# Performance work log

Measured on AMD Instinct MI355X. Metric: run time of the kernel, lower is better.

The kernel has to match this reference:

```python
import jax, jax.numpy as jnp
import numpy as np

B, S, E = 2, 4096, 768
NH, D = 12, 64
W = 256            # one-sided attention window (attention_window=512 // 2)
NEG = jnp.float32(-1e30)  # stands in for -inf at invalid band positions (safe grads)


def setup_inputs() -> dict:
    key = jax.random.key(0)
    ks = jax.random.split(key, 4)
    sc = 0.02
    return {
        'hidden_states': jax.random.normal(ks[0], (B, S, E), jnp.float32),
        'attention_mask': jnp.zeros((B, S), jnp.float32),   # 0 = local attention everywhere
        'is_index_masked': jnp.zeros((B, S), bool),
        'Wq': jax.random.normal(ks[1], (E, E), jnp.float32) * sc,
        'bq': jnp.zeros((E,), jnp.float32),
        'Wk': jax.random.normal(ks[2], (E, E), jnp.float32) * sc,
        'bk': jnp.zeros((E,), jnp.float32),
        'Wv': jax.random.normal(ks[3], (E, E), jnp.float32) * sc,
        'bv': jnp.zeros((E,), jnp.float32),
    }


def _longformer_local(hidden_states, attention_mask, is_index_masked, Wq, bq, Wk, bk, Wv, bv):
    b, s, e = hidden_states.shape
    w = W
    nc = s // w
    # projections (nn.Linear: x @ W.T + b); query pre-scaled by 1/sqrt(head_dim)
    q = (hidden_states @ Wq.T + bq) / jnp.sqrt(jnp.float32(D))
    k = hidden_states @ Wk.T + bk
    v = hidden_states @ Wv.T + bv
    # [B, NH, S, D]
    q = q.reshape(b, s, NH, D).transpose(0, 2, 1, 3)
    k = k.reshape(b, s, NH, D).transpose(0, 2, 1, 3)
    v = v.reshape(b, s, NH, D).transpose(0, 2, 1, 3)

    # pad keys/values by w on each side; chunk into [B,NH,nc,3w,D] windows
    kp = jnp.pad(k, ((0, 0), (0, 0), (w, w), (0, 0)))
    vp = jnp.pad(v, ((0, 0), (0, 0), (w, w), (0, 0)))
    starts = jnp.arange(nc) * w                      # [nc]
    cidx = starts[:, None] + jnp.arange(3 * w)[None, :]  # [nc, 3w] (padded coords)
    kc = kp[:, :, cidx, :]                            # [B,NH,nc,3w,D]
    vc = vp[:, :, cidx, :]                            # [B,NH,nc,3w,D]
    qc = q.reshape(b, NH, nc, w, D)

    # banded scores: query p in chunk attends keys at offsets p..p+2w within the 3w window
    scores = jnp.einsum('bhcpd,bhckd->bhcpk', qc, kc)  # [B,NH,nc,w,3w]
    p = jnp.arange(w)[:, None]
    koff = jnp.arange(2 * w + 1)[None, :]
    band_idx = p + koff                                # [w, 2w+1]
    band = jnp.take_along_axis(scores, band_idx[None, None, None], axis=-1)  # [B,NH,nc,w,2w+1]

    # additive mask from attention_mask (torch: finfo.min where !=0), gathered at key positions
    fmask = jnp.where(attention_mask != 0, jnp.finfo(jnp.float32).min, jnp.float32(0.0))  # [B,S]
    j = starts[:, None, None] + band_idx[None] - w     # global key index [nc,w,2w+1]
    valid = (j >= 0) & (j < s)
    jc = jnp.clip(j, 0, s - 1)
    band = band + fmask[:, jc][:, None]                # [B,1->NH,nc,w,2w+1]
    # _mask_invalid_locations: out-of-sequence band entries -> -inf (NEG)
    band = jnp.where(valid[None, None], band, NEG)

    probs = jax.nn.softmax(band.astype(jnp.float32), axis=-1)
    # zero probs at fully-masked query positions
    im = is_index_masked.reshape(b, 1, nc, w, 1)
    probs = jnp.where(im, jnp.float32(0.0), probs)

    # scatter band back to [B,NH,nc,w,3w] and contract with value chunks
    full = jnp.zeros((b, NH, nc, w, 3 * w), probs.dtype).at[:, :, :, p, band_idx].set(probs)
    out = jnp.einsum('bhcpk,bhckd->bhcpd', full, vc)   # [B,NH,nc,w,D]
    out = out.reshape(b, NH, s, D).transpose(0, 2, 1, 3).reshape(b, s, e)
    return out


def reference(hidden_states, attention_mask, is_index_masked, Wq, bq, Wk, bk, Wv, bv):
    return _longformer_local(hidden_states, attention_mask, is_index_masked,
                             Wq, bq, Wk, bk, Wv, bv)
```

## Files before the change

### kernel.cpp

```cpp
#include <hip/hip_runtime.h>

typedef __bf16 bf16;
typedef __attribute__((ext_vector_type(8))) __bf16 bf16x8;
typedef __attribute__((ext_vector_type(4))) __bf16 bf16x4;
typedef __attribute__((ext_vector_type(4))) float f32x4;

#define MFMA16(a, b, c) __builtin_amdgcn_mfma_f32_16x16x32_bf16((a), (b), (c), 0, 0, 0)

#define S_LEN 4096
#define NHEAD 12
#define EMB   768
#define NEGV  (-1e30f)

__device__ __forceinline__ void gload16(const bf16* g, bf16* l) {
  __builtin_amdgcn_global_load_lds((const __attribute__((address_space(1))) void*)g,
                                   (__attribute__((address_space(3))) void*)l, 16, 0, 0);
}

__global__ __launch_bounds__(256) void cvt_kernel(const float* __restrict__ x,
                                                  bf16* __restrict__ o, int n8, float scale) {
  int i = blockIdx.x * 256 + threadIdx.x;
  if (i >= n8) return;
  const float4* p = (const float4*)(x + (size_t)i * 8);
  float4 a = p[0], b = p[1];
  bf16x8 v;
  v[0] = (bf16)(a.x * scale); v[1] = (bf16)(a.y * scale);
  v[2] = (bf16)(a.z * scale); v[3] = (bf16)(a.w * scale);
  v[4] = (bf16)(b.x * scale); v[5] = (bf16)(b.y * scale);
  v[6] = (bf16)(b.z * scale); v[7] = (bf16)(b.w * scale);
  *(bf16x8*)(o + (size_t)i * 8) = v;
}

__global__ __launch_bounds__(256) void cvt3_kernel(const float* __restrict__ w0,
                                                   const float* __restrict__ w1,
                                                   const float* __restrict__ w2,
                                                   bf16* __restrict__ o, int n8) {
  int which = blockIdx.y;
  const float* src = (which == 0) ? w0 : (which == 1) ? w1 : w2;
  float scale = (which == 0) ? 0.125f : 1.0f;
  int i = blockIdx.x * 256 + threadIdx.x;
  if (i >= n8) return;
  const float4* p = (const float4*)(src + (size_t)i * 8);
  float4 a = p[0], b = p[1];
  bf16x8 v;
  v[0] = (bf16)(a.x * scale); v[1] = (bf16)(a.y * scale);
  v[2] = (bf16)(a.z * scale); v[3] = (bf16)(a.w * scale);
  v[4] = (bf16)(b.x * scale); v[5] = (bf16)(b.y * scale);
  v[6] = (bf16)(b.z * scale); v[7] = (bf16)(b.w * scale);
  *(bf16x8*)(o + ((size_t)which * n8 + i) * 8) = v;
}

__global__ __launch_bounds__(256) void qkv_gemm(const bf16* __restrict__ Xb, const bf16* __restrict__ Wb,
                                                const float* __restrict__ bq, const float* __restrict__ bk,
                                                const float* __restrict__ bv,
                                                bf16* __restrict__ Qo, bf16* __restrict__ Ko,
                                                bf16* __restrict__ Vt) {
  __shared__ union SM {
    struct { bf16 a[128 * 64]; bf16 b[128 * 64]; } st;
    bf16 c[128 * 130];
  } sm;
  const int tid = threadIdx.x;
  const int l = tid & 63, w = tid >> 6;
  const int ln = l & 15, g = l >> 4;
  const int wm = w >> 1, wn = w & 1;
  const int m0 = blockIdx.x * 128;
  const int n0 = blockIdx.y * 128;

  const f32x4 zero4 = {0.f, 0.f, 0.f, 0.f};
  f32x4 acc[4][4];
#pragma unroll
  for (int i = 0; i < 4; ++i)
#pragma unroll
    for (int j = 0; j < 4; ++j) acc[i][j] = zero4;

  for (int kt = 0; kt < 12; ++kt) {
    const int k0 = kt * 64;
#pragma unroll
    for (int i = 0; i < 4; ++i) {
      const int G = w * 256 + i * 64 + l;
      const int row = G >> 3, dsl = G & 7;
      const int slot = dsl ^ (row & 7);
      gload16(Xb + (size_t)(m0 + row) * 768 + k0 + slot * 8, &sm.st.a[(w * 256 + i * 64) * 8]);
      gload16(Wb + (size_t)(n0 + row) * 768 + k0 + slot * 8, &sm.st.b[(w * 256 + i * 64) * 8]);
    }
    asm volatile("s_waitcnt vmcnt(0)" ::: "memory");
    __syncthreads();
#pragma unroll
    for (int kc = 0; kc < 2; ++kc) {
      bf16x8 af[4], bfr[4];
#pragma unroll
      for (int i = 0; i < 4; ++i) {
        int ra = wm * 64 + i * 16 + ln;
        af[i] = *(const bf16x8*)(&sm.st.a[ra * 64 + ((kc * 4 + g) ^ (ra & 7)) * 8]);
        int rb = wn * 64 + i * 16 + ln;
        bfr[i] = *(const bf16x8*)(&sm.st.b[rb * 64 + ((kc * 4 + g) ^ (rb & 7)) * 8]);
      }
#pragma unroll
      for (int mi = 0; mi < 4; ++mi)
#pragma unroll
        for (int ni = 0; ni < 4; ++ni)
          acc[mi][ni] = MFMA16(af[mi], bfr[ni], acc[mi][ni]);
    }
    __syncthreads();
  }

  const int which = n0 / 768;
  const int h0 = (n0 % 768) >> 6;
  const int b = m0 >> 12;
  const int h = h0 + wn;
  const float bsc = (which == 0) ? 0.125f : 1.0f;
  const float* bias = (which == 0) ? bq : (which == 1) ? bk : bv;
  float bvv[4];
#pragma unroll
  for (int ni = 0; ni < 4; ++ni) bvv[ni] = bias[h * 64 + ni * 16 + ln] * bsc;

  if (which < 2) {
    bf16* dst = (which == 0) ? Qo : Ko;
    const size_t base = ((size_t)(b * NHEAD + h) * S_LEN + (m0 & 4095)) * 64;
#pragma unroll
    for (int mi = 0; mi < 4; ++mi)
#pragma unroll
      for (int ni = 0; ni < 4; ++ni)
#pragma unroll
        for (int r = 0; r < 4; ++r) {
          int sl = wm * 64 + mi * 16 + g * 4 + r;
          dst[base + (size_t)sl * 64 + ni * 16 + ln] = (bf16)(acc[mi][ni][r] + bvv[ni]);
        }
  } else {
#pragma unroll
    for (int mi = 0; mi < 4; ++mi)
#pragma unroll
      for (int ni = 0; ni < 4; ++ni)
#pragma unroll
        for (int r = 0; r < 4; ++r) {
          int sl = wm * 64 + mi * 16 + g * 4 + r;
          sm.c[sl * 130 + wn * 64 + ni * 16 + ln] = (bf16)(acc[mi][ni][r] + bvv[ni]);
        }
    __syncthreads();
#pragma unroll
    for (int it = 0; it < 4; ++it) {
      int d = it * 32 + (tid >> 3);
      int scp = tid & 7;
      int hh = h0 + (d >> 6);
      bf16x8 o0, o1;
#pragma unroll
      for (int i2 = 0; i2 < 8; ++i2) o0[i2] = sm.c[(scp * 16 + i2) * 130 + d];
#pragma unroll
      for (int i2 = 0; i2 < 8; ++i2) o1[i2] = sm.c[(scp * 16 + 8 + i2) * 130 + d];
      bf16* dp = Vt + ((size_t)(b * NHEAD + hh) * 64 + (d & 63)) * S_LEN + (m0 & 4095) + scp * 16;
      *(bf16x8*)dp = o0;
      *(bf16x8*)(dp + 8) = o1;
    }
  }
}

__global__ __launch_bounds__(512) void attn_kernel(const bf16* __restrict__ Qb, const bf16* __restrict__ Kb,
                                                   const bf16* __restrict__ Vtb,
                                                   const float* __restrict__ amask,
                                                   const unsigned char* __restrict__ imask,
                                                   float* __restrict__ out) {
  __shared__ bf16 Ks[2][64 * 64];
  __shared__ bf16 Vs[2][64 * 64];
  __shared__ bf16 Pt[8][16 * 64];
  __shared__ float Ams[2][64];
  const int tid = threadIdx.x;
  const int l = tid & 63, w = tid >> 6;
  const int ln = l & 15, g = l >> 4;
  const int orig = blockIdx.x;
  const int lb = (orig & 7) * 96 + (orig >> 3);
  const int qc = lb & 31, bh = lb >> 5;
  const int b = bh / NHEAD, h = bh % NHEAD;
  const int q0 = qc * 128;
  const int qg = q0 + w * 16 + ln;

  const size_t qoff = ((size_t)bh * S_LEN + qg) * 64;
  const bf16x8 qf0 = *(const bf16x8*)(Qb + qoff + g * 8);
  const bf16x8 qf1 = *(const bf16x8*)(Qb + qoff + 32 + g * 8);

  const f32x4 zero4 = {0.f, 0.f, 0.f, 0.f};
  f32x4 acc[4];
#pragma unroll
  for (int i = 0; i < 4; ++i) acc[i] = zero4;
  float mrun = -1e38f, lrun = 0.f;

  const int t_lo = (q0 >= 256) ? 0 : ((256 - q0) >> 6);
  int t_hi = (S_LEN + 256 - q0) >> 6;
  if (t_hi > 10) t_hi = 10;

  auto stage = [&](int sb, int t) {
    const int tj0 = q0 - 256 + t * 64;
    const int G = w * 64 + l;
    const int row = G >> 3, dsl = G & 7;
    const int slot = dsl ^ (row & 7);
    gload16(Kb + ((size_t)bh * S_LEN + tj0 + row) * 64 + slot * 8, &Ks[sb][w * 512]);
    gload16(Vtb + ((size_t)bh * 64 + row) * S_LEN + tj0 + slot * 8, &Vs[sb][w * 512]);
    if (tid < 64) {
      float am = amask[b * S_LEN + tj0 + tid];
      Ams[sb][tid] = (am != 0.f) ? -1e30f : 0.f;
    }
  };

  stage(0, t_lo);
  asm volatile("s_waitcnt vmcnt(0)" ::: "memory");
  __syncthreads();

  int buf = 0;
  for (int t = t_lo; t < t_hi; ++t, buf ^= 1) {
    if (t + 1 < t_hi) stage(buf ^ 1, t + 1);
    const int tj0 = q0 - 256 + t * 64;

    f32x4 sc[4];
#pragma unroll
    for (int i = 0; i < 4; ++i) sc[i] = zero4;
    __builtin_amdgcn_s_setprio(1);
#pragma unroll
    for (int kc = 0; kc < 2; ++kc) {
      bf16x8 qf = kc ? qf1 : qf0;
#pragma unroll
      for (int mi = 0; mi < 4; ++mi) {
        int r = mi * 16 + ln;
        bf16x8 kf = *(const bf16x8*)(&Ks[buf][r * 64 + ((kc * 4 + g) ^ (r & 7)) * 8]);
        sc[mi] = MFMA16(kf, qf, sc[mi]);
      }
    }
    __builtin_amdgcn_s_setprio(0);

    float mt = -1e38f;
    const bool full = (t * 64 >= w * 16 + 15) && (t * 64 <= w * 16 + 449);
    if (full) {
#pragma unroll
      for (int mi = 0; mi < 4; ++mi)
#pragma unroll
        for (int r = 0; r < 4; ++r) {
          int key = mi * 16 + g * 4 + r;
          float v = sc[mi][r] + Ams[buf][key];
          sc[mi][r] = v;
          mt = fmaxf(mt, v);
        }
    } else {
#pragma unroll
      for (int mi = 0; mi < 4; ++mi)
#pragma unroll
        for (int r = 0; r < 4; ++r) {
          int key = mi * 16 + g * 4 + r;
          int j = tj0 + key;
          bool valid = (j >= qg - 256) && (j <= qg + 256);
          float v = valid ? (sc[mi][r] + Ams[buf][key]) : NEGV;
          sc[mi][r] = v;
          mt = fmaxf(mt, v);
        }
    }
    mt = fmaxf(mt, __shfl_xor(mt, 16));
    mt = fmaxf(mt, __shfl_xor(mt, 32));
    if (!__all(mt <= mrun + 8.f)) {
      float mnew = fmaxf(mrun, mt);
      float corr = __expf(mrun - mnew);
      lrun *= corr;
#pragma unroll
      for (int i = 0; i < 4; ++i) acc[i] *= corr;
      mrun = mnew;
    }
    float psum = 0.f;
    float pv[4][4];
#pragma unroll
    for (int mi = 0; mi < 4; ++mi)
#pragma unroll
      for (int r = 0; r < 4; ++r) {
        float p = __expf(sc[mi][r] - mrun);
        pv[mi][r] = p;
        psum += p;
      }
    psum += __shfl_xor(psum, 16);
    psum += __shfl_xor(psum, 32);
    lrun += psum;

    bf16* PtW = &Pt[w][0];
#pragma unroll
    for (int mi = 0; mi < 4; ++mi) {
      bf16x4 pk;
      pk[0] = (bf16)pv[mi][0]; pk[1] = (bf16)pv[mi][1];
      pk[2] = (bf16)pv[mi][2]; pk[3] = (bf16)pv[mi][3];
      *(bf16x4*)(&PtW[ln * 64 + ((mi * 4 + g) ^ ln) * 4]) = pk;
    }

    __builtin_amdgcn_s_setprio(1);
#pragma unroll
    for (int ds2 = 0; ds2 < 4; ++ds2) {
#pragma unroll
      for (int kc = 0; kc < 2; ++kc) {
        int r = ds2 * 16 + ln;
        bf16x8 vf = *(const bf16x8*)(&Vs[buf][r * 64 + ((kc * 4 + g) ^ (r & 7)) * 8]);
        bf16x4 pa = *(const bf16x4*)(&PtW[ln * 64 + ((kc * 8 + g * 2) ^ ln) * 4]);
        bf16x4 pb = *(const bf16x4*)(&PtW[ln * 64 + ((kc * 8 + g * 2 + 1) ^ ln) * 4]);
        bf16x8 pf = __builtin_shufflevector(pa, pb, 0, 1, 2, 3, 4, 5, 6, 7);
        acc[ds2] = MFMA16(vf, pf, acc[ds2]);
      }
    }
    __builtin_amdgcn_s_setprio(0);

    asm volatile("s_waitcnt vmcnt(0)" ::: "memory");
    __syncthreads();
  }

  float rl = 1.0f / lrun;
  if (imask[b * S_LEN + qg] != 0) rl = 0.0f;
  float* ob = out + ((size_t)b * S_LEN + qg) * EMB + h * 64;
#pragma unroll
  for (int ds2 = 0; ds2 < 4; ++ds2) {
    float4 o;
    o.x = acc[ds2][0] * rl; o.y = acc[ds2][1] * rl;
    o.z = acc[ds2][2] * rl; o.w = acc[ds2][3] * rl;
    *(float4*)(ob + ds2 * 16 + g * 4) = o;
  }
}

extern "C" void kernel_launch(void* const* d_in, const int* in_sizes, int n_in,
                              void* d_out, int out_size, void* d_ws, size_t ws_size,
                              hipStream_t stream) {
  const float* X = (const float*)d_in[0];
  const float* amask = (const float*)d_in[1];
  const unsigned char* imask = (const unsigned char*)d_in[2];
  const float* Wq = (const float*)d_in[3];
  const float* bq = (const float*)d_in[4];
  const float* Wk = (const float*)d_in[5];
  const float* bk = (const float*)d_in[6];
  const float* Wv = (const float*)d_in[7];
  const float* bv = (const float*)d_in[8];
  float* out = (float*)d_out;

  bf16* Xb = (bf16*)d_ws;
  bf16* Wb = Xb + 6291456;
  bf16* Qb = Wb + 3 * 589824;
  bf16* Kb = Qb + 6291456;
  bf16* Vt = Kb + 6291456;

  cvt_kernel<<<3072, 256, 0, stream>>>(X, Xb, 6291456 / 8, 1.0f);
  cvt3_kernel<<<dim3(288, 3), 256, 0, stream>>>(Wq, Wk, Wv, Wb, 589824 / 8);
  qkv_gemm<<<dim3(64, 18), 256, 0, stream>>>(Xb, Wb, bq, bk, bv, Qb, Kb, Vt);
  attn_kernel<<<768, 512, 0, stream>>>(Qb, Kb, Vt, amask, imask, out);
}
```

Baseline: 186.3 us.

## Double-buffer QKV GEMM LDS tiles and stage Q/K epilogue through LDS

The QKV projection GEMM now keeps two LDS buffers for the A and B tiles. It issues the global-to-LDS loads for the next K-step before computing on the current one, so memory latency can overlap with MFMA work. The Q/K epilogue now also goes through the shared C tile, turning scattered 2-byte global stores into 16-byte row-contiguous writes. In exchange, LDS use doubles, which can lower occupancy. The explicit vmcnt wait was removed, so correctness relies on the barrier draining the async loads. The 130-element row pitch also makes the 16-byte LDS reads misaligned.

```diff
diff --git a/kernel.cpp b/kernel.cpp
--- a/kernel.cpp
+++ b/kernel.cpp
@@ -56,7 +56,7 @@
                                                 bf16* __restrict__ Qo, bf16* __restrict__ Ko,
                                                 bf16* __restrict__ Vt) {
   __shared__ union SM {
-    struct { bf16 a[128 * 64]; bf16 b[128 * 64]; } st;
+    struct { bf16 a[2][128 * 64]; bf16 b2[2][128 * 64]; } st;
     bf16 c[128 * 130];
   } sm;
   const int tid = threadIdx.x;
@@ -73,27 +73,38 @@
 #pragma unroll
     for (int j = 0; j < 4; ++j) acc[i][j] = zero4;
 
-  for (int kt = 0; kt < 12; ++kt) {
+  int srow[4], sslot[4];
+#pragma unroll
+  for (int i = 0; i < 4; ++i) {
+    const int G = w * 256 + i * 64 + l;
+    srow[i] = G >> 3;
+    sslot[i] = (G & 7) ^ (srow[i] & 7);
+  }
+
+  auto stage = [&](int sb, int kt) {
     const int k0 = kt * 64;
 #pragma unroll
     for (int i = 0; i < 4; ++i) {
-      const int G = w * 256 + i * 64 + l;
-      const int row = G >> 3, dsl = G & 7;
-      const int slot = dsl ^ (row & 7);
-      gload16(Xb + (size_t)(m0 + row) * 768 + k0 + slot * 8, &sm.st.a[(w * 256 + i * 64) * 8]);
-      gload16(Wb + (size_t)(n0 + row) * 768 + k0 + slot * 8, &sm.st.b[(w * 256 + i * 64) * 8]);
-    }
-    asm volatile("s_waitcnt vmcnt(0)" ::: "memory");
-    __syncthreads();
+      gload16(Xb + (size_t)(m0 + srow[i]) * 768 + k0 + sslot[i] * 8, &sm.st.a[sb][(w * 256 + i * 64) * 8]);
+      gload16(Wb + (size_t)(n0 + srow[i]) * 768 + k0 + sslot[i] * 8, &sm.st.b2[sb][(w * 256 + i * 64) * 8]);
+    }
+  };
+
+  stage(0, 0);
+  __syncthreads();
+
+  int buf = 0;
+  for (int kt = 0; kt < 12; ++kt, buf ^= 1) {
+    if (kt < 11) stage(buf ^ 1, kt + 1);
 #pragma unroll
     for (int kc = 0; kc < 2; ++kc) {
       bf16x8 af[4], bfr[4];
 #pragma unroll
       for (int i = 0; i < 4; ++i) {
         int ra = wm * 64 + i * 16 + ln;
-        af[i] = *(const bf16x8*)(&sm.st.a[ra * 64 + ((kc * 4 + g) ^ (ra & 7)) * 8]);
+        af[i] = *(const bf16x8*)(&sm.st.a[buf][ra * 64 + ((kc * 4 + g) ^ (ra & 7)) * 8]);
         int rb = wn * 64 + i * 16 + ln;
-        bfr[i] = *(const bf16x8*)(&sm.st.b[rb * 64 + ((kc * 4 + g) ^ (rb & 7)) * 8]);
+        bfr[i] = *(const bf16x8*)(&sm.st.b2[buf][rb * 64 + ((kc * 4 + g) ^ (rb & 7)) * 8]);
       }
 #pragma unroll
       for (int mi = 0; mi < 4; ++mi)
@@ -114,29 +125,28 @@
 #pragma unroll
   for (int ni = 0; ni < 4; ++ni) bvv[ni] = bias[h * 64 + ni * 16 + ln] * bsc;
 
+#pragma unroll
+  for (int mi = 0; mi < 4; ++mi)
+#pragma unroll
+    for (int ni = 0; ni < 4; ++ni)
+#pragma unroll
+      for (int r = 0; r < 4; ++r) {
+        int sl = wm * 64 + mi * 16 + g * 4 + r;
+        sm.c[sl * 130 + wn * 64 + ni * 16 + ln] = (bf16)(acc[mi][ni][r] + bvv[ni]);
+      }
+  __syncthreads();
+
   if (which < 2) {
     bf16* dst = (which == 0) ? Qo : Ko;
-    const size_t base = ((size_t)(b * NHEAD + h) * S_LEN + (m0 & 4095)) * 64;
-#pragma unroll
-    for (int mi = 0; mi < 4; ++mi)
-#pragma unroll
-      for (int ni = 0; ni < 4; ++ni)
-#pragma unroll
-        for (int r = 0; r < 4; ++r) {
-          int sl = wm * 64 + mi * 16 + g * 4 + r;
-          dst[base + (size_t)sl * 64 + ni * 16 + ln] = (bf16)(acc[mi][ni][r] + bvv[ni]);
-        }
+#pragma unroll
+    for (int it = 0; it < 8; ++it) {
+      int gid = it * 256 + tid;
+      int sl = gid >> 4, cg = gid & 15;
+      int hh = h0 + (cg >> 3);
+      bf16x8 v8 = *(const bf16x8*)(&sm.c[sl * 130 + cg * 8]);
+      *(bf16x8*)(dst + ((size_t)(b * NHEAD + hh) * S_LEN + (m0 & 4095) + sl) * 64 + (cg & 7) * 8) = v8;
+    }
   } else {
-#pragma unroll
-    for (int mi = 0; mi < 4; ++mi)
-#pragma unroll
-      for (int ni = 0; ni < 4; ++ni)
-#pragma unroll
-        for (int r = 0; r < 4; ++r) {
-          int sl = wm * 64 + mi * 16 + g * 4 + r;
-          sm.c[sl * 130 + wn * 64 + ni * 16 + ln] = (bf16)(acc[mi][ni][r] + bvv[ni]);
-        }
-    __syncthreads();
 #pragma unroll
     for (int it = 0; it < 4; ++it) {
       int d = it * 32 + (tid >> 3);
```

New measurement: 172.2 us. -7.5%, faster.
